# Performance work log

Measured on AMD Instinct MI355X. Metric: run time of the kernel, lower is better.

Reference implementation:

```python
import jax, jax.numpy as jnp
import numpy as np
import math

B, S, D, H = 2, 2048, 1024, 16
DK = D // H


def setup_inputs() -> dict:
    key = jax.random.key(0)
    ks = jax.random.split(key, 12)
    std = 1.0 / math.sqrt(D)
    inp = {
        "query": jax.random.normal(ks[0], (B, S, D), jnp.float32),
        "key": jax.random.normal(ks[1], (B, S, D), jnp.float32),
        "value": jax.random.normal(ks[2], (B, S, D), jnp.float32),
        # causal mask, broadcast over batch and heads
        "mask": jnp.tril(jnp.ones((S, S), jnp.int32))[None, None, :, :],
        # nn.Linear weights are [out_features, in_features]
        "Wq": jax.random.uniform(ks[3], (D, D), jnp.float32, -std, std),
        "bq": jax.random.uniform(ks[4], (D,), jnp.float32, -std, std),
        "Wk": jax.random.uniform(ks[5], (D, D), jnp.float32, -std, std),
        "bk": jax.random.uniform(ks[6], (D,), jnp.float32, -std, std),
        "Wv": jax.random.uniform(ks[7], (D, D), jnp.float32, -std, std),
        "bv": jax.random.uniform(ks[8], (D,), jnp.float32, -std, std),
        "Wo": jax.random.uniform(ks[9], (D, D), jnp.float32, -std, std),
        "bo": jax.random.uniform(ks[10], (D,), jnp.float32, -std, std),
    }
    return inp


def reference(query, key, value, mask, Wq, bq, Wk, bk, Wv, bv, Wo, bo):
    q = query @ Wq.T + bq  # [B,S,D]
    k = key @ Wk.T + bk
    v = value @ Wv.T + bv
    # Faithful to the original: a raw view (reshape), NOT a head-transpose split.
    q = q.reshape(B, H, S, DK)
    k = k.reshape(B, H, S, DK)
    v = v.reshape(B, H, S, DK)
    scores = jnp.einsum("bhqd,bhkd->bhqk", q, k) / math.sqrt(DK)
    scores = jnp.where(mask == 0, jnp.float32(-1e9), scores)
    weights = jax.nn.softmax(scores, axis=-1)
    # dropout(p=0.1) is identity in eval mode
    context = jnp.einsum("bhqk,bhkd->bhqd", weights, v)
    context = context.transpose(0, 2, 1, 3).reshape(B, S, D)
    return context @ Wo.T + bo
```

## Files before the change

kernel.cpp:

```cpp
#include <hip/hip_runtime.h>
#include <hip/hip_bf16.h>

#define BB 2
#define SS 2048
#define DD 1024
#define HH 16
#define DKK 64

typedef __attribute__((ext_vector_type(4))) float  f32x4;
typedef __attribute__((ext_vector_type(8))) short  s16x8;
typedef __attribute__((ext_vector_type(4))) short  s16x4;
typedef __attribute__((ext_vector_type(4))) float  fvec4;

__device__ __forceinline__ short f2bs(float f) {
    union { __hip_bfloat16 b; short s; } u;
    u.b = __float2bfloat16(f);
    return u.s;
}

__device__ __forceinline__ void gload_lds16(const short* g, short* l) {
    __builtin_amdgcn_global_load_lds((const __attribute__((address_space(1))) void*)g,
                                     (__attribute__((address_space(3))) void*)l, 16, 0, 0);
}

__global__ __launch_bounds__(256) void cvt_all(
    const float* __restrict__ q,  const float* __restrict__ k,  const float* __restrict__ v,
    const float* __restrict__ wq, const float* __restrict__ wk, const float* __restrict__ wv,
    const float* __restrict__ wo,
    short* __restrict__ qo,  short* __restrict__ ko,  short* __restrict__ vo,
    short* __restrict__ wqo, short* __restrict__ wko, short* __restrict__ wvo,
    short* __restrict__ woo)
{
    const float* src; short* dst; int n;
    switch (blockIdx.y) {
        case 0: src = q;  dst = qo;  n = BB * SS * DD; break;
        case 1: src = k;  dst = ko;  n = BB * SS * DD; break;
        case 2: src = v;  dst = vo;  n = BB * SS * DD; break;
        case 3: src = wq; dst = wqo; n = DD * DD; break;
        case 4: src = wk; dst = wko; n = DD * DD; break;
        case 5: src = wv; dst = wvo; n = DD * DD; break;
        default: src = wo; dst = woo; n = DD * DD; break;
    }
    int i = (blockIdx.x * 256 + threadIdx.x) * 8;
    const int stride = gridDim.x * 256 * 8;
    for (; i < n; i += stride) {
        fvec4 a = *(const fvec4*)&src[i];
        fvec4 b = *(const fvec4*)&src[i + 4];
        s16x8 o;
        o[0] = f2bs(a[0]); o[1] = f2bs(a[1]); o[2] = f2bs(a[2]); o[3] = f2bs(a[3]);
        o[4] = f2bs(b[0]); o[5] = f2bs(b[1]); o[6] = f2bs(b[2]); o[7] = f2bs(b[3]);
        *(s16x8*)&dst[i] = o;
    }
}

template<int BN, bool OUTF32>
__global__ __launch_bounds__(256) void gemm_nt_bf16(
    const short* __restrict__ A0, const short* __restrict__ A1, const short* __restrict__ A2,
    const short* __restrict__ B0, const short* __restrict__ B1, const short* __restrict__ B2,
    const float* __restrict__ c0, const float* __restrict__ c1, const float* __restrict__ c2,
    void* __restrict__ O0, void* __restrict__ O1, void* __restrict__ O2,
    float os0, float os1, float os2, int M, int N, int K)
{
    const int z = blockIdx.z;
    const short* A    = z == 0 ? A0 : (z == 1 ? A1 : A2);
    const short* Bw   = z == 0 ? B0 : (z == 1 ? B1 : B2);
    const float* bias = z == 0 ? c0 : (z == 1 ? c1 : c2);
    void* Cp          = z == 0 ? O0 : (z == 1 ? O1 : O2);
    const float oscale = z == 0 ? os0 : (z == 1 ? os1 : os2);

    __shared__ short As[128][32];
    __shared__ short Bs[BN][32];

    const int tid  = threadIdx.x;
    const int lane = tid & 63;
    const int wid  = tid >> 6;
    const int r16  = lane & 15;
    const int g    = lane >> 4;
    const int m0   = blockIdx.y * 128;
    const int n0   = blockIdx.x * BN;
    constexpr int MR = (BN == 128) ? 4 : 2;
    constexpr int NR = 4;
    const int wr = (BN == 128) ? (wid >> 1) * 64 : wid * 32;
    const int wc = (BN == 128) ? (wid & 1) * 64 : 0;
    const int lrow = lane >> 2;
    const int lch  = (lane & 3) * 8;

    f32x4 acc[MR][NR];
#pragma unroll
    for (int mi = 0; mi < MR; ++mi)
#pragma unroll
        for (int ni = 0; ni < NR; ++ni) acc[mi][ni] = (f32x4){0.f, 0.f, 0.f, 0.f};

    const int nk = K >> 5;
#pragma unroll 1
    for (int kt = 0; kt < nk; ++kt) {
        const int k0 = kt * 32;
        if (kt) __syncthreads();
        {
            const short* ga = &A[(size_t)(m0 + wid * 32 + lrow) * K + k0 + lch];
            gload_lds16(ga, &As[wid * 32][0]);
            gload_lds16(ga + (size_t)16 * K, &As[wid * 32 + 16][0]);
        }
        if constexpr (BN == 128) {
            const short* gb = &Bw[(size_t)(n0 + wid * 32 + lrow) * K + k0 + lch];
            gload_lds16(gb, &Bs[wid * 32][0]);
            gload_lds16(gb + (size_t)16 * K, &Bs[wid * 32 + 16][0]);
        } else {
            const short* gb = &Bw[(size_t)(n0 + wid * 16 + lrow) * K + k0 + lch];
            gload_lds16(gb, &Bs[wid * 16][0]);
        }
        __syncthreads();

        s16x8 af[MR], bf[NR];
#pragma unroll
        for (int mi = 0; mi < MR; ++mi)
            af[mi] = *(const s16x8*)&As[wr + mi * 16 + r16][g * 8];
#pragma unroll
        for (int ni = 0; ni < NR; ++ni)
            bf[ni] = *(const s16x8*)&Bs[wc + ni * 16 + r16][g * 8];
#pragma unroll
        for (int mi = 0; mi < MR; ++mi)
#pragma unroll
            for (int ni = 0; ni < NR; ++ni)
                acc[mi][ni] = __builtin_amdgcn_mfma_f32_16x16x32_bf16(
                    af[mi], bf[ni], acc[mi][ni], 0, 0, 0);
    }

#pragma unroll
    for (int ni = 0; ni < NR; ++ni) {
        const int col = n0 + wc + ni * 16 + r16;
        const float bv = bias[col];
#pragma unroll
        for (int mi = 0; mi < MR; ++mi) {
#pragma unroll
            for (int r = 0; r < 4; ++r) {
                const int row = m0 + wr + mi * 16 + g * 4 + r;
                const float vv = (acc[mi][ni][r] + bv) * oscale;
                if constexpr (OUTF32)
                    ((float*)Cp)[(size_t)row * N + col] = vv;
                else
                    ((short*)Cp)[(size_t)row * N + col] = f2bs(vv);
            }
        }
    }
}

__global__ __launch_bounds__(256) void mha_transpose_v(
    const short* __restrict__ vp, short* __restrict__ vT)
{
    const int st = blockIdx.x;
    const int bh = blockIdx.y;
    const short* src = vp + (size_t)bh * SS * DKK;
    short*       dst = vT + (size_t)bh * SS * DKK;
    const int tid = threadIdx.x;
#pragma unroll
    for (int i = 0; i < 2; ++i) {
        const int c  = tid + i * 256;
        const int dk = c >> 3;
        const int sc = c & 7;
        const int s0 = st * 64 + sc * 8;
        s16x8 v;
#pragma unroll
        for (int j = 0; j < 8; ++j) v[j] = src[(size_t)(s0 + j) * DKK + dk];
        *(s16x8*)&dst[(size_t)dk * SS + s0] = v;
    }
}

__global__ __launch_bounds__(256, 2) void mha_attn(
    const short* __restrict__ qp, const short* __restrict__ kp,
    const short* __restrict__ vT, short* __restrict__ ctx)
{
    __shared__ short Ks[64][64];
    __shared__ short Vs[64][64];
    __shared__ short P[4][16][72];

    const int tid  = threadIdx.x;
    const int wid  = tid >> 6;
    const int lane = tid & 63;
    const int r16  = lane & 15;
    const int g    = lane >> 4;

    const int bh  = blockIdx.x;
    const int bxp = blockIdx.y;
    const int b   = bh >> 4;
    const int h   = bh & 15;

    const short* Qh = qp + (size_t)bh * SS * DKK;
    const short* Kh = kp + (size_t)bh * SS * DKK;
    const short* Vh = vT + (size_t)bh * SS * DKK;

    const int srow = lane >> 3;
    const int r0   = wid * 16;

#pragma unroll 1
    for (int t = 0; t < 2; ++t) {
        const int grp = t ? (31 - bxp) : bxp;
        const int qr0 = grp * 64 + wid * 16;
        const int nkt = grp + 1;

        const s16x8 qf0 = *(const s16x8*)&Qh[(size_t)(qr0 + r16) * DKK + g * 8];
        const s16x8 qf1 = *(const s16x8*)&Qh[(size_t)(qr0 + r16) * DKK + 32 + g * 8];

        f32x4 po[4];
#pragma unroll
        for (int i = 0; i < 4; ++i) po[i] = (f32x4){0.f, 0.f, 0.f, 0.f};
        float l_[4] = {0.f, 0.f, 0.f, 0.f};

#pragma unroll 1
        for (int j = 0; j < nkt; ++j) {
            const int k0 = j * 64;
            __syncthreads();
            {
                const int rowA = r0 + srow;
                const int rowB = rowA + 8;
                const int cA = (((lane & 7) ^ (rowA & 7)) & 7) * 8;
                const int cB = (((lane & 7) ^ (rowB & 7)) & 7) * 8;
                gload_lds16(&Kh[(size_t)(k0 + rowA) * DKK + cA], &Ks[r0][0]);
                gload_lds16(&Kh[(size_t)(k0 + rowB) * DKK + cB], &Ks[r0 + 8][0]);
                gload_lds16(&Vh[(size_t)rowA * SS + k0 + cA], &Vs[r0][0]);
                gload_lds16(&Vh[(size_t)rowB * SS + k0 + cB], &Vs[r0 + 8][0]);
            }
            __syncthreads();

            f32x4 sc[4];
            __builtin_amdgcn_s_setprio(1);
#pragma unroll
            for (int cg = 0; cg < 4; ++cg) {
                const int R  = cg * 16 + r16;
                const int sw = R & 7;
                const s16x8 kf0 = *(const s16x8*)&Ks[R][((g ^ sw) & 7) * 8];
                const s16x8 kf1 = *(const s16x8*)&Ks[R][(((4 + g) ^ sw) & 7) * 8];
                f32x4 tt = (f32x4){0.f, 0.f, 0.f, 0.f};
                tt = __builtin_amdgcn_mfma_f32_16x16x32_bf16(qf0, kf0, tt, 0, 0, 0);
                tt = __builtin_amdgcn_mfma_f32_16x16x32_bf16(qf1, kf1, tt, 0, 0, 0);
                sc[cg] = tt;
            }
            __builtin_amdgcn_s_setprio(0);

            if (j == nkt - 1) {
#pragma unroll
                for (int cg = 0; cg < 4; ++cg)
#pragma unroll
                    for (int r = 0; r < 4; ++r)
                        if (k0 + cg * 16 + r16 > qr0 + g * 4 + r) sc[cg][r] = -1e9f;
            }
#pragma unroll
            for (int cg = 0; cg < 4; ++cg)
#pragma unroll
                for (int r = 0; r < 4; ++r) {
                    const float p = __expf(sc[cg][r]);
                    l_[r] += p;
                    P[wid][g * 4 + r][cg * 16 + r16] = f2bs(p);
                }
            const s16x8 pf0 = *(const s16x8*)&P[wid][r16][g * 8];
            const s16x8 pf1 = *(const s16x8*)&P[wid][r16][32 + g * 8];

            __builtin_amdgcn_s_setprio(1);
#pragma unroll
            for (int dg = 0; dg < 4; ++dg) {
                const int Rv = dg * 16 + r16;
                const int sw = Rv & 7;
                const s16x8 vf0 = *(const s16x8*)&Vs[Rv][((g ^ sw) & 7) * 8];
                const s16x8 vf1 = *(const s16x8*)&Vs[Rv][(((4 + g) ^ sw) & 7) * 8];
                po[dg] = __builtin_amdgcn_mfma_f32_16x16x32_bf16(pf0, vf0, po[dg], 0, 0, 0);
                po[dg] = __builtin_amdgcn_mfma_f32_16x16x32_bf16(pf1, vf1, po[dg], 0, 0, 0);
            }
            __builtin_amdgcn_s_setprio(0);
        }

#pragma unroll
        for (int r = 0; r < 4; ++r) {
#pragma unroll
            for (int off = 1; off < 16; off <<= 1)
                l_[r] += __shfl_xor(l_[r], off);
        }
#pragma unroll
        for (int dg = 0; dg < 4; ++dg)
#pragma unroll
            for (int r = 0; r < 4; ++r) {
                const int srw = qr0 + g * 4 + r;
                const float v = po[dg][r] * __builtin_amdgcn_rcpf(l_[r]);
                ctx[((size_t)(b * SS + srw)) * DD + h * 64 + dg * 16 + r16] = f2bs(v);
            }
    }
}

extern "C" void kernel_launch(void* const* d_in, const int* in_sizes, int n_in,
                              void* d_out, int out_size, void* d_ws, size_t ws_size,
                              hipStream_t stream) {
    const float* query = (const float*)d_in[0];
    const float* key   = (const float*)d_in[1];
    const float* value = (const float*)d_in[2];
    const float* Wq = (const float*)d_in[4];
    const float* bq = (const float*)d_in[5];
    const float* Wk = (const float*)d_in[6];
    const float* bk = (const float*)d_in[7];
    const float* Wv = (const float*)d_in[8];
    const float* bv = (const float*)d_in[9];
    const float* Wo = (const float*)d_in[10];
    const float* bo = (const float*)d_in[11];
    float* out = (float*)d_out;

    const size_t elems = (size_t)BB * SS * DD;
    const size_t wel   = (size_t)DD * DD;
    short* qx  = (short*)d_ws;
    short* kx  = qx + elems;
    short* vx  = kx + elems;
    short* wqx = vx + elems;
    short* wkx = wqx + wel;
    short* wvx = wkx + wel;
    short* wox = wvx + wel;
    short* qp  = wox + wel;
    short* kp  = qp + elems;
    short* vp  = kp + elems;
    short* vT  = qx;
    short* ctx = kx;

    const int M = BB * SS;

    cvt_all<<<dim3(1024, 7), 256, 0, stream>>>(query, key, value, Wq, Wk, Wv, Wo,
                                               qx, kx, vx, wqx, wkx, wvx, wox);
    gemm_nt_bf16<128, false><<<dim3(DD / 128, M / 128, 3), 256, 0, stream>>>(
        qx, kx, vx, wqx, wkx, wvx, bq, bk, bv, qp, kp, vp,
        0.125f, 1.0f, 1.0f, M, DD, DD);
    mha_transpose_v<<<dim3(SS / 64, BB * HH), 256, 0, stream>>>(vp, vT);
    mha_attn<<<dim3(BB * HH, 16), 256, 0, stream>>>(qp, kp, vT, ctx);
    gemm_nt_bf16<64, true><<<dim3(DD / 64, M / 128, 1), 256, 0, stream>>>(
        ctx, ctx, ctx, wox, wox, wox, bo, bo, bo, out, out, out,
        1.0f, 1.0f, 1.0f, M, DD, DD);
}
```

Before: 125.8 us.

## Rework GEMMs with BK=64 swizzled LDS, XCD-aware tile mapping, split-K output projection

Replaces the projection GEMM with a version that loads 64-wide K tiles into XOR-swizzled shared memory and maps blocks to XCDs so that tiles sharing panels land on the same die. The output projection now uses 128x128 tiles with a two-way split-K into float partial buffers, followed by a combine kernel that adds the partials and the bias. The aim is fewer barriers per K step, fewer LDS bank conflicts, better L2 locality and more blocks for the output GEMM. In exchange it adds an extra elementwise pass that reads and writes large float partials, and it reuses workspace buffers for those partials.

```diff
diff --git a/kernel.cpp b/kernel.cpp
--- a/kernel.cpp
+++ b/kernel.cpp
@@ -53,85 +53,99 @@
     }
 }
 
-template<int BN, bool OUTF32>
-__global__ __launch_bounds__(256) void gemm_nt_bf16(
+template<bool OUTF32>
+__global__ __launch_bounds__(256) void gemm_nt_v2(
     const short* __restrict__ A0, const short* __restrict__ A1, const short* __restrict__ A2,
     const short* __restrict__ B0, const short* __restrict__ B1, const short* __restrict__ B2,
     const float* __restrict__ c0, const float* __restrict__ c1, const float* __restrict__ c2,
     void* __restrict__ O0, void* __restrict__ O1, void* __restrict__ O2,
-    float os0, float os1, float os2, int M, int N, int K)
-{
-    const int z = blockIdx.z;
+    float os0, float os1, float os2,
+    int ko0, int ko1, int ko2,
+    int ppx, int NY, int KL, int N, int K)
+{
+    const int d   = blockIdx.x;
+    const int xcd = d & 7;
+    const int s   = d >> 3;
+    const int x   = s & 7;
+    const int pl  = s >> 3;
+    const int panel = xcd * ppx + pl;
+    const int y   = panel % NY;
+    const int z   = panel / NY;
+
     const short* A    = z == 0 ? A0 : (z == 1 ? A1 : A2);
     const short* Bw   = z == 0 ? B0 : (z == 1 ? B1 : B2);
     const float* bias = z == 0 ? c0 : (z == 1 ? c1 : c2);
     void* Cp          = z == 0 ? O0 : (z == 1 ? O1 : O2);
     const float oscale = z == 0 ? os0 : (z == 1 ? os1 : os2);
-
-    __shared__ short As[128][32];
-    __shared__ short Bs[BN][32];
+    const int koff     = z == 0 ? ko0 : (z == 1 ? ko1 : ko2);
+
+    __shared__ short As[128][64];
+    __shared__ short Bs[128][64];
 
     const int tid  = threadIdx.x;
     const int lane = tid & 63;
     const int wid  = tid >> 6;
     const int r16  = lane & 15;
     const int g    = lane >> 4;
-    const int m0   = blockIdx.y * 128;
-    const int n0   = blockIdx.x * BN;
-    constexpr int MR = (BN == 128) ? 4 : 2;
-    constexpr int NR = 4;
-    const int wr = (BN == 128) ? (wid >> 1) * 64 : wid * 32;
-    const int wc = (BN == 128) ? (wid & 1) * 64 : 0;
-    const int lrow = lane >> 2;
-    const int lch  = (lane & 3) * 8;
-
-    f32x4 acc[MR][NR];
-#pragma unroll
-    for (int mi = 0; mi < MR; ++mi)
-#pragma unroll
-        for (int ni = 0; ni < NR; ++ni) acc[mi][ni] = (f32x4){0.f, 0.f, 0.f, 0.f};
-
-    const int nk = K >> 5;
+    const int m0   = y * 128;
+    const int n0   = x * 128;
+    const int wr   = (wid >> 1) * 64;
+    const int wc   = (wid & 1) * 64;
+    const int srow8 = lane >> 3;
+    const int c8    = lane & 7;
+
+    f32x4 acc[4][4];
+#pragma unroll
+    for (int mi = 0; mi < 4; ++mi)
+#pragma unroll
+        for (int ni = 0; ni < 4; ++ni) acc[mi][ni] = (f32x4){0.f, 0.f, 0.f, 0.f};
+
+    const int csrc = (c8 ^ srow8) * 8;
+    const int nk = KL >> 6;
 #pragma unroll 1
     for (int kt = 0; kt < nk; ++kt) {
-        const int k0 = kt * 32;
+        const int k0 = koff + kt * 64;
         if (kt) __syncthreads();
-        {
-            const short* ga = &A[(size_t)(m0 + wid * 32 + lrow) * K + k0 + lch];
-            gload_lds16(ga, &As[wid * 32][0]);
-            gload_lds16(ga + (size_t)16 * K, &As[wid * 32 + 16][0]);
-        }
-        if constexpr (BN == 128) {
-            const short* gb = &Bw[(size_t)(n0 + wid * 32 + lrow) * K + k0 + lch];
-            gload_lds16(gb, &Bs[wid * 32][0]);
-            gload_lds16(gb + (size_t)16 * K, &Bs[wid * 32 + 16][0]);
-        } else {
-            const short* gb = &Bw[(size_t)(n0 + wid * 16 + lrow) * K + k0 + lch];
-            gload_lds16(gb, &Bs[wid * 16][0]);
+#pragma unroll
+        for (int q = 0; q < 4; ++q) {
+            const int r = wid * 32 + q * 8 + srow8;
+            gload_lds16(&A[(size_t)(m0 + r) * K + k0 + csrc], &As[wid * 32 + q * 8][0]);
+        }
+#pragma unroll
+        for (int q = 0; q < 4; ++q) {
+            const int r = wid * 32 + q * 8 + srow8;
+            gload_lds16(&Bw[(size_t)(n0 + r) * K + k0 + csrc], &Bs[wid * 32 + q * 8][0]);
         }
         __syncthreads();
 
-        s16x8 af[MR], bf[NR];
-#pragma unroll
-        for (int mi = 0; mi < MR; ++mi)
-            af[mi] = *(const s16x8*)&As[wr + mi * 16 + r16][g * 8];
-#pragma unroll
-        for (int ni = 0; ni < NR; ++ni)
-            bf[ni] = *(const s16x8*)&Bs[wc + ni * 16 + r16][g * 8];
-#pragma unroll
-        for (int mi = 0; mi < MR; ++mi)
-#pragma unroll
-            for (int ni = 0; ni < NR; ++ni)
-                acc[mi][ni] = __builtin_amdgcn_mfma_f32_16x16x32_bf16(
-                    af[mi], bf[ni], acc[mi][ni], 0, 0, 0);
-    }
-
-#pragma unroll
-    for (int ni = 0; ni < NR; ++ni) {
+#pragma unroll
+        for (int kk = 0; kk < 2; ++kk) {
+            s16x8 af[4], bf[4];
+#pragma unroll
+            for (int mi = 0; mi < 4; ++mi) {
+                const int row = wr + mi * 16 + r16;
+                af[mi] = *(const s16x8*)&As[row][((kk * 4 + g) ^ (row & 7)) * 8];
+            }
+#pragma unroll
+            for (int ni = 0; ni < 4; ++ni) {
+                const int row = wc + ni * 16 + r16;
+                bf[ni] = *(const s16x8*)&Bs[row][((kk * 4 + g) ^ (row & 7)) * 8];
+            }
+#pragma unroll
+            for (int mi = 0; mi < 4; ++mi)
+#pragma unroll
+                for (int ni = 0; ni < 4; ++ni)
+                    acc[mi][ni] = __builtin_amdgcn_mfma_f32_16x16x32_bf16(
+                        af[mi], bf[ni], acc[mi][ni], 0, 0, 0);
+        }
+    }
+
+#pragma unroll
+    for (int ni = 0; ni < 4; ++ni) {
         const int col = n0 + wc + ni * 16 + r16;
-        const float bv = bias[col];
-#pragma unroll
-        for (int mi = 0; mi < MR; ++mi) {
+        const float bv = bias ? bias[col] : 0.f;
+#pragma unroll
+        for (int mi = 0; mi < 4; ++mi) {
 #pragma unroll
             for (int r = 0; r < 4; ++r) {
                 const int row = m0 + wr + mi * 16 + g * 4 + r;
@@ -142,6 +156,27 @@
                     ((short*)Cp)[(size_t)row * N + col] = f2bs(vv);
             }
         }
+    }
+}
+
+__global__ __launch_bounds__(256) void combine_o(
+    const float* __restrict__ P0, const float* __restrict__ P1,
+    const float* __restrict__ bo, float* __restrict__ out)
+{
+    const int n = BB * SS * DD;
+    int i = (blockIdx.x * 256 + threadIdx.x) * 8;
+    const int stride = gridDim.x * 256 * 8;
+    for (; i < n; i += stride) {
+        fvec4 a0 = *(const fvec4*)&P0[i];
+        fvec4 a1 = *(const fvec4*)&P0[i + 4];
+        fvec4 b0 = *(const fvec4*)&P1[i];
+        fvec4 b1 = *(const fvec4*)&P1[i + 4];
+        fvec4 c0 = *(const fvec4*)&bo[i & (DD - 1)];
+        fvec4 c1 = *(const fvec4*)&bo[(i + 4) & (DD - 1)];
+        fvec4 o0 = a0 + b0 + c0;
+        fvec4 o1 = a1 + b1 + c1;
+        *(fvec4*)&out[i] = o0;
+        *(fvec4*)&out[i + 4] = o1;
     }
 }
 
@@ -314,18 +349,22 @@
     short* kp  = qp + elems;
     short* vp  = kp + elems;
     short* vT  = qx;
-    short* ctx = kx;
+    short* ctx = vx;
+    float* P0  = (float*)qx;
+    float* P1  = (float*)qp;
 
     const int M = BB * SS;
 
     cvt_all<<<dim3(1024, 7), 256, 0, stream>>>(query, key, value, Wq, Wk, Wv, Wo,
                                                qx, kx, vx, wqx, wkx, wvx, wox);
-    gemm_nt_bf16<128, false><<<dim3(DD / 128, M / 128, 3), 256, 0, stream>>>(
+    gemm_nt_v2<false><<<dim3(768), 256, 0, stream>>>(
         qx, kx, vx, wqx, wkx, wvx, bq, bk, bv, qp, kp, vp,
-        0.125f, 1.0f, 1.0f, M, DD, DD);
+        0.125f, 1.0f, 1.0f, 0, 0, 0, 12, 32, 1024, DD, DD);
     mha_transpose_v<<<dim3(SS / 64, BB * HH), 256, 0, stream>>>(vp, vT);
     mha_attn<<<dim3(BB * HH, 16), 256, 0, stream>>>(qp, kp, vT, ctx);
-    gemm_nt_bf16<64, true><<<dim3(DD / 64, M / 128, 1), 256, 0, stream>>>(
-        ctx, ctx, ctx, wox, wox, wox, bo, bo, bo, out, out, out,
-        1.0f, 1.0f, 1.0f, M, DD, DD);
-}
+    gemm_nt_v2<true><<<dim3(512), 256, 0, stream>>>(
+        ctx, ctx, ctx, wox, wox, wox, nullptr, nullptr, nullptr,
+        (void*)P0, (void*)P1, (void*)P1,
+        1.0f, 1.0f, 1.0f, 0, 512, 512, 8, 32, 512, DD, DD);
+    combine_o<<<dim3(2048), 256, 0, stream>>>(P0, P1, bo, out);
+}
```

Measured after the change: 128.5 us. 2.1% more time.
